# Performance work log

Hardware: AMD Instinct MI355X
Metric: run time of the kernel (lower is better)

## Reference

```python
import jax, jax.numpy as jnp
import numpy as np

D_MODEL = 1024
N_HEADS = 16
D_K = D_MODEL // N_HEADS


def setup_inputs() -> dict:
    key = jax.random.key(0)
    ks = jax.random.split(key, 9)
    s = 1.0 / np.sqrt(D_MODEL)
    x = jax.random.normal(ks[0], (2, 2048, D_MODEL), dtype=jnp.float32)
    Wq = jax.random.normal(ks[1], (D_MODEL, D_MODEL), dtype=jnp.float32) * s
    bq = jnp.zeros((D_MODEL,), jnp.float32)
    Wk = jax.random.normal(ks[2], (D_MODEL, D_MODEL), dtype=jnp.float32) * s
    bk = jnp.zeros((D_MODEL,), jnp.float32)
    Wv = jax.random.normal(ks[3], (D_MODEL, D_MODEL), dtype=jnp.float32) * s
    bv = jnp.zeros((D_MODEL,), jnp.float32)
    Wo = jax.random.normal(ks[4], (D_MODEL, D_MODEL), dtype=jnp.float32) * s
    bo = jnp.zeros((D_MODEL,), jnp.float32)
    return {"x": x, "Wq": Wq, "bq": bq, "Wk": Wk, "bk": bk,
            "Wv": Wv, "bv": bv, "Wo": Wo, "bo": bo}


def reference(x, Wq, bq, Wk, bk, Wv, bv, Wo, bo):
    B, T, C = x.shape
    H, Dk = N_HEADS, D_K
    # QKV projections, reshape to [B, H, T, Dk]
    q = (x @ Wq + bq).reshape(B, T, H, Dk).transpose(0, 2, 1, 3)
    k = (x @ Wk + bk).reshape(B, T, H, Dk).transpose(0, 2, 1, 3)
    v = (x @ Wv + bv).reshape(B, T, H, Dk).transpose(0, 2, 1, 3)
    scale = 1.0 / np.sqrt(Dk).astype(np.float32)
    att = jnp.einsum('bhqd,bhkd->bhqk', q, k) * scale  # [B,H,T,T]
    causal = jnp.tril(jnp.ones((T, T), dtype=bool))
    att = jnp.where(causal, att, -jnp.inf)
    att = jax.nn.softmax(att, axis=-1)
    y = jnp.einsum('bhqk,bhkd->bhqd', att, v)  # [B,H,T,Dk]
    y = y.transpose(0, 2, 1, 3).reshape(B, T, C)
    return y @ Wo + bo
```

## Files before the change

kernel.cpp:

```cpp
#include <hip/hip_runtime.h>
#include <stdint.h>

#define D_MODEL 1024
#define N_HEADS 16
#define D_K     64
#define T_SEQ   2048
#define BATCH   2
#define M_TOT   (BATCH * T_SEQ)
#define QCH     128

typedef __attribute__((ext_vector_type(8))) short  short8;
typedef __attribute__((ext_vector_type(4))) float  f32x4;
typedef __attribute__((ext_vector_type(4))) unsigned short u16x4;

typedef __attribute__((address_space(1))) void gvoid;
typedef __attribute__((address_space(3))) void lvoid;

#define QSCALE 0.18033688011112042f

static __device__ __forceinline__ unsigned short f2bf(float f) {
    union { float f; unsigned u; } v; v.f = f;
    unsigned u = v.u;
    u += 0x7fffu + ((u >> 16) & 1u);
    return (unsigned short)(u >> 16);
}
static __device__ __forceinline__ float bf2f(unsigned short s) {
    union { unsigned u; float f; } v; v.u = ((unsigned)s) << 16;
    return v.f;
}
static __device__ __forceinline__ float fexp2(float x) {
    float r;
    asm("v_exp_f32 %0, %1" : "=v"(r) : "v"(x));
    return r;
}
static __device__ __forceinline__ unsigned cvt_pk_bf16(float lo, float hi) {
    unsigned r;
    asm("v_cvt_pk_bf16_f32 %0, %1, %2" : "=v"(r) : "v"(lo), "v"(hi));
    return r;
}

__global__ void cvt_x(const float* __restrict__ in, unsigned short* __restrict__ out) {
    int idx = blockIdx.x * blockDim.x + threadIdx.x;
    const float4* in4 = (const float4*)in;
    float4 v = in4[idx];
    u16x4 o;
    o.x = f2bf(v.x); o.y = f2bf(v.y); o.z = f2bf(v.z); o.w = f2bf(v.w);
    *(u16x4*)&out[(size_t)idx * 4] = o;
}

__global__ void cvt_w_t(const float* w0, const float* w1, const float* w2, const float* w3,
                        unsigned short* o0, unsigned short* o1, unsigned short* o2, unsigned short* o3) {
    const float* w; unsigned short* o;
    switch (blockIdx.z) {
        case 0: w = w0; o = o0; break;
        case 1: w = w1; o = o1; break;
        case 2: w = w2; o = o2; break;
        default: w = w3; o = o3; break;
    }
    __shared__ float tile[32][33];
    int n0 = blockIdx.x * 32, k0 = blockIdx.y * 32;
    int tx = threadIdx.x, ty = threadIdx.y;
    #pragma unroll
    for (int r = 0; r < 32; r += 8)
        tile[ty + r][tx] = w[(size_t)(k0 + ty + r) * D_MODEL + n0 + tx];
    __syncthreads();
    #pragma unroll
    for (int r = 0; r < 32; r += 8)
        o[(size_t)(n0 + ty + r) * D_MODEL + k0 + tx] = f2bf(tile[tx][ty + r]);
}

__global__ __launch_bounds__(256) void gemm_qkv(const unsigned short* __restrict__ A,
                                                const unsigned short* __restrict__ wq,
                                                const unsigned short* __restrict__ wk,
                                                const unsigned short* __restrict__ wv,
                                                const float* __restrict__ bq,
                                                const float* __restrict__ bk,
                                                const float* __restrict__ bv,
                                                unsigned short* __restrict__ qo,
                                                unsigned short* __restrict__ ko,
                                                unsigned short* __restrict__ vo) {
    const int z = blockIdx.z;
    const unsigned short* Bt = (z == 0) ? wq : (z == 1) ? wk : wv;
    const float* bias = (z == 0) ? bq : (z == 1) ? bk : bv;
    const float alpha = (z == 0) ? QSCALE : 1.0f;

    __shared__ unsigned short lA[128 * 32];
    __shared__ unsigned short lB[128 * 32];
    const int tid  = threadIdx.x;
    const int w    = tid >> 6, lane = tid & 63;
    const int tm   = blockIdx.y, tn = blockIdx.x;
    const int wm   = w & 1, wn = w >> 1;
    const int i16  = lane & 15, g4 = lane >> 4;
    f32x4 acc[4][4] = {};

    const int rA0 = tm * 128, rB0 = tn * 128;
    const int srow = lane >> 2;
    const int skc  = (lane & 3) * 8;

    for (int k0 = 0; k0 < D_MODEL; k0 += 32) {
        #pragma unroll
        for (int is = 0; is < 2; ++is) {
            int c   = is * 4 + w;
            int row = c * 16 + srow;
            __builtin_amdgcn_global_load_lds(
                (gvoid*)(A + (size_t)(rA0 + row) * D_MODEL + k0 + skc),
                (lvoid*)&lA[c * 512], 16, 0, 0);
            __builtin_amdgcn_global_load_lds(
                (gvoid*)(Bt + (size_t)(rB0 + row) * D_MODEL + k0 + skc),
                (lvoid*)&lB[c * 512], 16, 0, 0);
        }
        __syncthreads();
        short8 af[4], bfr[4];
        #pragma unroll
        for (int mi = 0; mi < 4; ++mi)
            af[mi] = *(const short8*)&lA[(wm * 64 + mi * 16 + i16) * 32 + g4 * 8];
        #pragma unroll
        for (int ni = 0; ni < 4; ++ni)
            bfr[ni] = *(const short8*)&lB[(wn * 64 + ni * 16 + i16) * 32 + g4 * 8];
        #pragma unroll
        for (int mi = 0; mi < 4; ++mi)
            #pragma unroll
            for (int ni = 0; ni < 4; ++ni)
                acc[mi][ni] = __builtin_amdgcn_mfma_f32_16x16x32_bf16(af[mi], bfr[ni], acc[mi][ni], 0, 0, 0);
        __syncthreads();
    }

    #pragma unroll
    for (int mi = 0; mi < 4; ++mi)
        #pragma unroll
        for (int ni = 0; ni < 4; ++ni) {
            int col = tn * 128 + wn * 64 + ni * 16 + i16;
            float bv2 = bias[col];
            #pragma unroll
            for (int r = 0; r < 4; ++r) {
                int row = tm * 128 + wm * 64 + mi * 16 + g4 * 4 + r;
                float val = (acc[mi][ni][r] + bv2) * alpha;
                int b = row >> 11, t = row & (T_SEQ - 1);
                int h = col >> 6,  d = col & (D_K - 1);
                unsigned short bfv = f2bf(val);
                if (z == 2)
                    vo[(((size_t)(b * N_HEADS + h)) * D_K + d) * T_SEQ + t] = bfv;
                else if (z == 1)
                    ko[(((size_t)(b * N_HEADS + h)) * T_SEQ + t) * D_K + d] = bfv;
                else
                    qo[(((size_t)(b * N_HEADS + h)) * T_SEQ + t) * D_K + d] = bfv;
            }
        }
}

__global__ __launch_bounds__(256) void gemm_out(const unsigned short* __restrict__ A,
                                                const unsigned short* __restrict__ Bt,
                                                const float* __restrict__ bias,
                                                float* __restrict__ Cout) {
    __shared__ unsigned short lA[128 * 32];
    __shared__ unsigned short lB[128 * 32];
    const int tid  = threadIdx.x;
    const int w    = tid >> 6, lane = tid & 63;
    const int tm   = blockIdx.y, tn = blockIdx.x;
    const int wm   = w & 1, wn = w >> 1;
    const int i16  = lane & 15, g4 = lane >> 4;
    f32x4 acc[4][4] = {};

    const int rA0 = tm * 128, rB0 = tn * 128;
    const int srow = lane >> 2;
    const int skc  = (lane & 3) * 8;

    for (int k0 = 0; k0 < D_MODEL; k0 += 32) {
        #pragma unroll
        for (int is = 0; is < 2; ++is) {
            int c   = is * 4 + w;
            int row = c * 16 + srow;
            __builtin_amdgcn_global_load_lds(
                (gvoid*)(A + (size_t)(rA0 + row) * D_MODEL + k0 + skc),
                (lvoid*)&lA[c * 512], 16, 0, 0);
            __builtin_amdgcn_global_load_lds(
                (gvoid*)(Bt + (size_t)(rB0 + row) * D_MODEL + k0 + skc),
                (lvoid*)&lB[c * 512], 16, 0, 0);
        }
        __syncthreads();
        short8 af[4], bfr[4];
        #pragma unroll
        for (int mi = 0; mi < 4; ++mi)
            af[mi] = *(const short8*)&lA[(wm * 64 + mi * 16 + i16) * 32 + g4 * 8];
        #pragma unroll
        for (int ni = 0; ni < 4; ++ni)
            bfr[ni] = *(const short8*)&lB[(wn * 64 + ni * 16 + i16) * 32 + g4 * 8];
        #pragma unroll
        for (int mi = 0; mi < 4; ++mi)
            #pragma unroll
            for (int ni = 0; ni < 4; ++ni)
                acc[mi][ni] = __builtin_amdgcn_mfma_f32_16x16x32_bf16(af[mi], bfr[ni], acc[mi][ni], 0, 0, 0);
        __syncthreads();
    }

    #pragma unroll
    for (int mi = 0; mi < 4; ++mi)
        #pragma unroll
        for (int ni = 0; ni < 4; ++ni) {
            int col = tn * 128 + wn * 64 + ni * 16 + i16;
            float bv2 = bias[col];
            #pragma unroll
            for (int r = 0; r < 4; ++r) {
                int row = tm * 128 + wm * 64 + mi * 16 + g4 * 4 + r;
                Cout[(size_t)row * D_MODEL + col] = acc[mi][ni][r] + bv2;
            }
        }
}

__global__ __launch_bounds__(256) void flash4(const unsigned short* __restrict__ q,
                                              const unsigned short* __restrict__ k,
                                              const unsigned short* __restrict__ vt,
                                              unsigned short* __restrict__ opart,
                                              float* __restrict__ lws) {
    __shared__ unsigned short lK[2][128 * 64];
    __shared__ unsigned short lV[2][64 * 128];
    __shared__ unsigned short lP[4][16 * 64];
    const int tid  = threadIdx.x;
    const int w    = tid >> 6, lane = tid & 63;
    const int i16  = lane & 15, g4 = lane >> 4;
    const int l8   = lane & 7,  g8 = lane >> 3;
    const int bx   = blockIdx.x;
    const int h    = bx & 1;
    const int bh   = (bx >> 1) & 31;
    const int p    = bx >> 6;

    const unsigned short* kp = k  + (size_t)bh * T_SEQ * D_K;
    const unsigned short* vp = vt + (size_t)bh * D_K * T_SEQ;
    unsigned short* Pw = &lP[w][0];
    const int swz  = (i16 & 7) << 3;
    const int ksrc = (l8 ^ g8) << 3;

    const int b = bh >> 4, hh = bh & 15;
    unsigned short* op = opart + (size_t)h * ((size_t)M_TOT * D_MODEL);

    auto stage = [&](int buf, int t128) {
        const int kvb = t128 * 128;
        #pragma unroll
        for (int i = 0; i < 4; ++i) {
            const int ch  = w * 4 + i;
            const int row = ch * 8 + g8;
            __builtin_amdgcn_global_load_lds(
                (gvoid*)(kp + (size_t)(kvb + row) * D_K + ksrc),
                (lvoid*)&lK[buf][ch * 512], 16, 0, 0);
        }
        #pragma unroll
        for (int i = 0; i < 4; ++i) {
            const int ch  = w * 4 + i;
            const int row = ch * 4 + (lane >> 4);
            const int u   = (lane & 15) ^ (row & 7);
            __builtin_amdgcn_global_load_lds(
                (gvoid*)(vp + (size_t)row * T_SEQ + kvb + u * 8),
                (lvoid*)&lV[buf][ch * 512], 16, 0, 0);
        }
    };

    #pragma unroll 1
    for (int ci = 0; ci < 2; ++ci) {
        const int c   = ci ? p : (15 - p);
        const int q0w = c * QCH + w * 32;
        const int cnt = (c >= h) ? ((c - h) >> 1) + 1 : 0;

        const unsigned short* qp = q + ((size_t)bh * T_SEQ + q0w) * D_K;
        short8 qf[2][2];
        #pragma unroll
        for (int qt = 0; qt < 2; ++qt)
            #pragma unroll
            for (int ks = 0; ks < 2; ++ks)
                qf[qt][ks] = *(const short8*)&qp[(qt * 16 + i16) * D_K + ks * 32 + g4 * 8];

        f32x4 o[2][4] = {};
        float l[2] = {0.f, 0.f};

        if (cnt > 0) stage(0, h);
        __syncthreads();

        for (int it = 0; it < cnt; ++it) {
            const int cur = it & 1;
            const int t   = h + 2 * it;
            if (it + 1 < cnt) stage(cur ^ 1, t + 2);

            #pragma unroll
            for (int sub = 0; sub < 2; ++sub) {
                const int kv0 = t * 128 + sub * 64;
                if (kv0 > q0w + 31) continue;
                const bool act0 = (kv0 <= q0w + 15);
                const unsigned short* Kc = &lK[cur][sub * 64 * 64];

                f32x4 s[4][2] = {};
                __builtin_amdgcn_s_setprio(1);
                #pragma unroll
                for (int ks = 0; ks < 2; ++ks)
                    #pragma unroll
                    for (int kt = 0; kt < 4; ++kt) {
                        short8 ka = *(const short8*)&Kc[(kt * 16 + i16) * 64 + ((ks * 32 + g4 * 8) ^ swz)];
                        if (act0)
                            s[kt][0] = __builtin_amdgcn_mfma_f32_16x16x32_bf16(ka, qf[0][ks], s[kt][0], 0, 0, 0);
                        s[kt][1] = __builtin_amdgcn_mfma_f32_16x16x32_bf16(ka, qf[1][ks], s[kt][1], 0, 0, 0);
                    }
                __builtin_amdgcn_s_setprio(0);

                #pragma unroll
                for (int qt = 0; qt < 2; ++qt) {
                    if (qt == 0 && !act0) continue;
                    const int qrow = q0w + qt * 16 + i16;
                    const bool diag = (kv0 + 63 > q0w + qt * 16);
                    float ps = 0.f;
                    unsigned pk[8];
                    #pragma unroll
                    for (int kt = 0; kt < 4; ++kt) {
                        f32x4 sc = s[kt][qt];
                        if (diag) {
                            #pragma unroll
                            for (int r = 0; r < 4; ++r)
                                if (kv0 + kt * 16 + g4 * 4 + r > qrow) sc[r] = -3e38f;
                        }
                        float p0 = fexp2(sc[0]), p1 = fexp2(sc[1]);
                        float p2 = fexp2(sc[2]), p3 = fexp2(sc[3]);
                        ps += (p0 + p1) + (p2 + p3);
                        pk[kt * 2]     = cvt_pk_bf16(p0, p1);
                        pk[kt * 2 + 1] = cvt_pk_bf16(p2, p3);
                    }
                    l[qt] += ps;
                    #pragma unroll
                    for (int kt = 0; kt < 4; ++kt) {
                        uint2 v2; v2.x = pk[kt * 2]; v2.y = pk[kt * 2 + 1];
                        *(uint2*)&Pw[i16 * 64 + ((kt * 16 + g4 * 4) ^ swz)] = v2;
                    }
                    short8 pB0 = *(const short8*)&Pw[i16 * 64 + (( 0 + g4 * 8) ^ swz)];
                    short8 pB1 = *(const short8*)&Pw[i16 * 64 + ((32 + g4 * 8) ^ swz)];
                    __builtin_amdgcn_s_setprio(1);
                    #pragma unroll
                    for (int dt = 0; dt < 4; ++dt) {
                        short8 va0 = *(const short8*)&lV[cur][(dt * 16 + i16) * 128 + ((sub * 64 +  0 + g4 * 8) ^ swz)];
                        short8 va1 = *(const short8*)&lV[cur][(dt * 16 + i16) * 128 + ((sub * 64 + 32 + g4 * 8) ^ swz)];
                        o[qt][dt] = __builtin_amdgcn_mfma_f32_16x16x32_bf16(va0, pB0, o[qt][dt], 0, 0, 0);
                        o[qt][dt] = __builtin_amdgcn_mfma_f32_16x16x32_bf16(va1, pB1, o[qt][dt], 0, 0, 0);
                    }
                    __builtin_amdgcn_s_setprio(0);
                }
            }
            __syncthreads();
        }

        #pragma unroll
        for (int qt = 0; qt < 2; ++qt) {
            float lt = l[qt] + __shfl_xor(l[qt], 16);
            lt += __shfl_xor(lt, 32);
            const int trow = q0w + qt * 16 + i16;
            if (g4 == 0)
                lws[((size_t)h * 32 + bh) * T_SEQ + trow] = lt;
            #pragma unroll
            for (int dt = 0; dt < 4; ++dt) {
                u16x4 ov;
                ov.x = f2bf(o[qt][dt][0]);
                ov.y = f2bf(o[qt][dt][1]);
                ov.z = f2bf(o[qt][dt][2]);
                ov.w = f2bf(o[qt][dt][3]);
                *(u16x4*)&op[((size_t)(b * T_SEQ) + trow) * D_MODEL + hh * D_K + dt * 16 + g4 * 4] = ov;
            }
        }
    }
}

__global__ __launch_bounds__(256) void merge_halves(const unsigned short* __restrict__ op,
                                                    const float* __restrict__ lws,
                                                    unsigned short* __restrict__ y) {
    const int idx = blockIdx.x * 256 + threadIdx.x;
    const int gl  = idx * 8;
    const int row = gl >> 10;
    const int col = gl & 1023;
    const int b = row >> 11, t = row & (T_SEQ - 1), h = col >> 6;
    const float l0 = lws[((size_t)(b * 16 + h)) * T_SEQ + t];
    const float l1 = lws[((size_t)(32 + b * 16 + h)) * T_SEQ + t];
    const float inv = 1.0f / (l0 + l1);
    short8 a = *(const short8*)&op[gl];
    short8 cc = *(const short8*)&op[(size_t)M_TOT * D_MODEL + gl];
    short8 r;
    #pragma unroll
    for (int j = 0; j < 8; ++j) {
        float f = bf2f((unsigned short)a[j]) + bf2f((unsigned short)cc[j]);
        r[j] = (short)f2bf(f * inv);
    }
    *(short8*)&y[gl] = r;
}

extern "C" void kernel_launch(void* const* d_in, const int* in_sizes, int n_in,
                              void* d_out, int out_size, void* d_ws, size_t ws_size,
                              hipStream_t stream) {
    const float* x  = (const float*)d_in[0];
    const float* Wq = (const float*)d_in[1];
    const float* bq = (const float*)d_in[2];
    const float* Wk = (const float*)d_in[3];
    const float* bk = (const float*)d_in[4];
    const float* Wv = (const float*)d_in[5];
    const float* bv = (const float*)d_in[6];
    const float* Wo = (const float*)d_in[7];
    const float* bo = (const float*)d_in[8];

    uint8_t* ws = (uint8_t*)d_ws;
    const size_t MB = (size_t)1 << 20;
    unsigned short* xb  = (unsigned short*)(ws);
    unsigned short* wqt = (unsigned short*)(ws + 8  * MB);
    unsigned short* wkt = (unsigned short*)(ws + 10 * MB);
    unsigned short* wvt = (unsigned short*)(ws + 12 * MB);
    unsigned short* wot = (unsigned short*)(ws + 14 * MB);
    unsigned short* qb  = (unsigned short*)(ws + 16 * MB);
    unsigned short* kb  = (unsigned short*)(ws + 24 * MB);
    unsigned short* vtb = (unsigned short*)(ws + 32 * MB);
    float* lws = (float*)(ws + 8 * MB);

    cvt_x<<<4096, 256, 0, stream>>>(x, xb);
    cvt_w_t<<<dim3(32, 32, 4), dim3(32, 8), 0, stream>>>(Wq, Wk, Wv, Wo, wqt, wkt, wvt, wot);

    dim3 ggrid(D_MODEL / 128, M_TOT / 128, 3);
    gemm_qkv<<<ggrid, 256, 0, stream>>>(xb, wqt, wkt, wvt, bq, bk, bv, qb, kb, vtb);

    flash4<<<512, 256, 0, stream>>>(qb, kb, vtb, (unsigned short*)d_out, lws);
    merge_halves<<<2048, 256, 0, stream>>>((const unsigned short*)d_out, lws, xb);

    gemm_out<<<dim3(D_MODEL / 128, M_TOT / 128), 256, 0, stream>>>(xb, wot, bo, (float*)d_out);
}
```

Measured before the change: 121.3 us.

## Run both causal query chunks concurrently in 512-thread flash blocks; remap GEMM blocks

The attention kernel now launches 512-thread blocks. Eight waves handle the two paired query chunks (c and 15-c) at the same time instead of one after the other, and they share 64-row K/V tiles loaded once per iteration. Waves whose causal range has ended sit idle at the barriers. Both GEMMs switch to a 1D grid whose block index is remapped so that consecutive blocks land on different XCDs. This is meant to improve L2 locality and spread load across the chiplets, with the risk of more barrier overhead per KV tile.

```diff
diff --git a/kernel.cpp b/kernel.cpp
--- a/kernel.cpp
+++ b/kernel.cpp
@@ -79,7 +79,12 @@
                                                 unsigned short* __restrict__ qo,
                                                 unsigned short* __restrict__ ko,
                                                 unsigned short* __restrict__ vo) {
-    const int z = blockIdx.z;
+    const int nb   = (blockIdx.x & 7) * 96 + (blockIdx.x >> 3);
+    const int tn   = nb & 7;
+    const int rest = nb >> 3;
+    const int tm   = rest & 31;
+    const int z    = rest >> 5;
+
     const unsigned short* Bt = (z == 0) ? wq : (z == 1) ? wk : wv;
     const float* bias = (z == 0) ? bq : (z == 1) ? bk : bv;
     const float alpha = (z == 0) ? QSCALE : 1.0f;
@@ -88,7 +93,6 @@
     __shared__ unsigned short lB[128 * 32];
     const int tid  = threadIdx.x;
     const int w    = tid >> 6, lane = tid & 63;
-    const int tm   = blockIdx.y, tn = blockIdx.x;
     const int wm   = w & 1, wn = w >> 1;
     const int i16  = lane & 15, g4 = lane >> 4;
     f32x4 acc[4][4] = {};
@@ -152,11 +156,14 @@
                                                 const unsigned short* __restrict__ Bt,
                                                 const float* __restrict__ bias,
                                                 float* __restrict__ Cout) {
+    const int nb = (blockIdx.x & 7) * 32 + (blockIdx.x >> 3);
+    const int tn = nb & 7;
+    const int tm = nb >> 3;
+
     __shared__ unsigned short lA[128 * 32];
     __shared__ unsigned short lB[128 * 32];
     const int tid  = threadIdx.x;
     const int w    = tid >> 6, lane = tid & 63;
-    const int tm   = blockIdx.y, tn = blockIdx.x;
     const int wm   = w & 1, wn = w >> 1;
     const int i16  = lane & 15, g4 = lane >> 4;
     f32x4 acc[4][4] = {};
@@ -207,157 +214,142 @@
         }
 }
 
-__global__ __launch_bounds__(256) void flash4(const unsigned short* __restrict__ q,
-                                              const unsigned short* __restrict__ k,
-                                              const unsigned short* __restrict__ vt,
-                                              unsigned short* __restrict__ opart,
-                                              float* __restrict__ lws) {
-    __shared__ unsigned short lK[2][128 * 64];
-    __shared__ unsigned short lV[2][64 * 128];
-    __shared__ unsigned short lP[4][16 * 64];
+__global__ __launch_bounds__(512, 4) void flash5(const unsigned short* __restrict__ q,
+                                                 const unsigned short* __restrict__ k,
+                                                 const unsigned short* __restrict__ vt,
+                                                 unsigned short* __restrict__ opart,
+                                                 float* __restrict__ lws) {
+    __shared__ unsigned short lK[2][64 * 64];
+    __shared__ unsigned short lV[2][64 * 64];
+    __shared__ unsigned short lP[8][16 * 64];
     const int tid  = threadIdx.x;
     const int w    = tid >> 6, lane = tid & 63;
     const int i16  = lane & 15, g4 = lane >> 4;
     const int l8   = lane & 7,  g8 = lane >> 3;
-    const int bx   = blockIdx.x;
-    const int h    = bx & 1;
-    const int bh   = (bx >> 1) & 31;
-    const int p    = bx >> 6;
+
+    const int nb = (blockIdx.x & 7) * 64 + (blockIdx.x >> 3);
+    const int p  = nb & 7;
+    const int h  = (nb >> 3) & 1;
+    const int bh = nb >> 4;
+    const int w4 = w & 3;
+    const int c  = (w >> 2) ? p : (15 - p);
+    const int q0w = c * QCH + w4 * 32;
+    const int cnt = 16 - p;
 
     const unsigned short* kp = k  + (size_t)bh * T_SEQ * D_K;
     const unsigned short* vp = vt + (size_t)bh * D_K * T_SEQ;
+    const unsigned short* qp = q  + ((size_t)bh * T_SEQ + q0w) * D_K;
     unsigned short* Pw = &lP[w][0];
-    const int swz  = (i16 & 7) << 3;
-    const int ksrc = (l8 ^ g8) << 3;
+    const int swz = (i16 & 7) << 3;
+
+    const int srow = tid >> 3;
+    const int sco  = (l8 ^ g8) << 3;
+
+    short8 qf[2][2];
+    #pragma unroll
+    for (int qt = 0; qt < 2; ++qt)
+        #pragma unroll
+        for (int ks = 0; ks < 2; ++ks)
+            qf[qt][ks] = *(const short8*)&qp[(qt * 16 + i16) * D_K + ks * 32 + g4 * 8];
+
+    f32x4 o[2][4] = {};
+    float l[2] = {0.f, 0.f};
+
+    auto stage = [&](int buf, int kv0s) {
+        __builtin_amdgcn_global_load_lds(
+            (gvoid*)(kp + (size_t)(kv0s + srow) * D_K + sco),
+            (lvoid*)&lK[buf][(size_t)tid * 8], 16, 0, 0);
+        __builtin_amdgcn_global_load_lds(
+            (gvoid*)(vp + (size_t)srow * T_SEQ + kv0s + sco),
+            (lvoid*)&lV[buf][(size_t)tid * 8], 16, 0, 0);
+    };
+
+    stage(0, h * 64);
+    __syncthreads();
+
+    for (int it = 0; it < cnt; ++it) {
+        const int cur = it & 1;
+        const int kv0 = (h + 2 * it) * 64;
+        if (it + 1 < cnt) stage(cur ^ 1, kv0 + 128);
+
+        if (kv0 <= q0w + 31) {
+            const bool act0 = (kv0 <= q0w + 15);
+            const unsigned short* Kc = &lK[cur][0];
+            const unsigned short* Vc = &lV[cur][0];
+
+            f32x4 s[4][2] = {};
+            __builtin_amdgcn_s_setprio(1);
+            #pragma unroll
+            for (int ks = 0; ks < 2; ++ks)
+                #pragma unroll
+                for (int kt = 0; kt < 4; ++kt) {
+                    short8 ka = *(const short8*)&Kc[(kt * 16 + i16) * 64 + ((ks * 32 + g4 * 8) ^ swz)];
+                    if (act0)
+                        s[kt][0] = __builtin_amdgcn_mfma_f32_16x16x32_bf16(ka, qf[0][ks], s[kt][0], 0, 0, 0);
+                    s[kt][1] = __builtin_amdgcn_mfma_f32_16x16x32_bf16(ka, qf[1][ks], s[kt][1], 0, 0, 0);
+                }
+            __builtin_amdgcn_s_setprio(0);
+
+            #pragma unroll
+            for (int qt = 0; qt < 2; ++qt) {
+                if (qt == 0 && !act0) continue;
+                const int qrow = q0w + qt * 16 + i16;
+                const bool diag = (kv0 + 63 > q0w + qt * 16);
+                float ps = 0.f;
+                unsigned pk[8];
+                #pragma unroll
+                for (int kt = 0; kt < 4; ++kt) {
+                    f32x4 sc = s[kt][qt];
+                    if (diag) {
+                        #pragma unroll
+                        for (int r = 0; r < 4; ++r)
+                            if (kv0 + kt * 16 + g4 * 4 + r > qrow) sc[r] = -3e38f;
+                    }
+                    float p0 = fexp2(sc[0]), p1 = fexp2(sc[1]);
+                    float p2 = fexp2(sc[2]), p3 = fexp2(sc[3]);
+                    ps += (p0 + p1) + (p2 + p3);
+                    pk[kt * 2]     = cvt_pk_bf16(p0, p1);
+                    pk[kt * 2 + 1] = cvt_pk_bf16(p2, p3);
+                }
+                l[qt] += ps;
+                #pragma unroll
+                for (int kt = 0; kt < 4; ++kt) {
+                    uint2 v2; v2.x = pk[kt * 2]; v2.y = pk[kt * 2 + 1];
+                    *(uint2*)&Pw[i16 * 64 + ((kt * 16 + g4 * 4) ^ swz)] = v2;
+                }
+                short8 pB0 = *(const short8*)&Pw[i16 * 64 + (( 0 + g4 * 8) ^ swz)];
+                short8 pB1 = *(const short8*)&Pw[i16 * 64 + ((32 + g4 * 8) ^ swz)];
+                __builtin_amdgcn_s_setprio(1);
+                #pragma unroll
+                for (int dt = 0; dt < 4; ++dt) {
+                    short8 va0 = *(const short8*)&Vc[(dt * 16 + i16) * 64 + (( 0 + g4 * 8) ^ swz)];
+                    short8 va1 = *(const short8*)&Vc[(dt * 16 + i16) * 64 + ((32 + g4 * 8) ^ swz)];
+                    o[qt][dt] = __builtin_amdgcn_mfma_f32_16x16x32_bf16(va0, pB0, o[qt][dt], 0, 0, 0);
+                    o[qt][dt] = __builtin_amdgcn_mfma_f32_16x16x32_bf16(va1, pB1, o[qt][dt], 0, 0, 0);
+                }
+                __builtin_amdgcn_s_setprio(0);
+            }
+        }
+        __syncthreads();
+    }
 
     const int b = bh >> 4, hh = bh & 15;
     unsigned short* op = opart + (size_t)h * ((size_t)M_TOT * D_MODEL);
-
-    auto stage = [&](int buf, int t128) {
-        const int kvb = t128 * 128;
-        #pragma unroll
-        for (int i = 0; i < 4; ++i) {
-            const int ch  = w * 4 + i;
-            const int row = ch * 8 + g8;
-            __builtin_amdgcn_global_load_lds(
-                (gvoid*)(kp + (size_t)(kvb + row) * D_K + ksrc),
-                (lvoid*)&lK[buf][ch * 512], 16, 0, 0);
-        }
-        #pragma unroll
-        for (int i = 0; i < 4; ++i) {
-            const int ch  = w * 4 + i;
-            const int row = ch * 4 + (lane >> 4);
-            const int u   = (lane & 15) ^ (row & 7);
-            __builtin_amdgcn_global_load_lds(
-                (gvoid*)(vp + (size_t)row * T_SEQ + kvb + u * 8),
-                (lvoid*)&lV[buf][ch * 512], 16, 0, 0);
-        }
-    };
-
-    #pragma unroll 1
-    for (int ci = 0; ci < 2; ++ci) {
-        const int c   = ci ? p : (15 - p);
-        const int q0w = c * QCH + w * 32;
-        const int cnt = (c >= h) ? ((c - h) >> 1) + 1 : 0;
-
-        const unsigned short* qp = q + ((size_t)bh * T_SEQ + q0w) * D_K;
-        short8 qf[2][2];
-        #pragma unroll
-        for (int qt = 0; qt < 2; ++qt)
-            #pragma unroll
-            for (int ks = 0; ks < 2; ++ks)
-                qf[qt][ks] = *(const short8*)&qp[(qt * 16 + i16) * D_K + ks * 32 + g4 * 8];
-
-        f32x4 o[2][4] = {};
-        float l[2] = {0.f, 0.f};
-
-        if (cnt > 0) stage(0, h);
-        __syncthreads();
-
-        for (int it = 0; it < cnt; ++it) {
-            const int cur = it & 1;
-            const int t   = h + 2 * it;
-            if (it + 1 < cnt) stage(cur ^ 1, t + 2);
-
-            #pragma unroll
-            for (int sub = 0; sub < 2; ++sub) {
-                const int kv0 = t * 128 + sub * 64;
-                if (kv0 > q0w + 31) continue;
-                const bool act0 = (kv0 <= q0w + 15);
-                const unsigned short* Kc = &lK[cur][sub * 64 * 64];
-
-                f32x4 s[4][2] = {};
-                __builtin_amdgcn_s_setprio(1);
-                #pragma unroll
-                for (int ks = 0; ks < 2; ++ks)
-                    #pragma unroll
-                    for (int kt = 0; kt < 4; ++kt) {
-                        short8 ka = *(const short8*)&Kc[(kt * 16 + i16) * 64 + ((ks * 32 + g4 * 8) ^ swz)];
-                        if (act0)
-                            s[kt][0] = __builtin_amdgcn_mfma_f32_16x16x32_bf16(ka, qf[0][ks], s[kt][0], 0, 0, 0);
-                        s[kt][1] = __builtin_amdgcn_mfma_f32_16x16x32_bf16(ka, qf[1][ks], s[kt][1], 0, 0, 0);
-                    }
-                __builtin_amdgcn_s_setprio(0);
-
-                #pragma unroll
-                for (int qt = 0; qt < 2; ++qt) {
-                    if (qt == 0 && !act0) continue;
-                    const int qrow = q0w + qt * 16 + i16;
-                    const bool diag = (kv0 + 63 > q0w + qt * 16);
-                    float ps = 0.f;
-                    unsigned pk[8];
-                    #pragma unroll
-                    for (int kt = 0; kt < 4; ++kt) {
-                        f32x4 sc = s[kt][qt];
-                        if (diag) {
-                            #pragma unroll
-                            for (int r = 0; r < 4; ++r)
-                                if (kv0 + kt * 16 + g4 * 4 + r > qrow) sc[r] = -3e38f;
-                        }
-                        float p0 = fexp2(sc[0]), p1 = fexp2(sc[1]);
-                        float p2 = fexp2(sc[2]), p3 = fexp2(sc[3]);
-                        ps += (p0 + p1) + (p2 + p3);
-                        pk[kt * 2]     = cvt_pk_bf16(p0, p1);
-                        pk[kt * 2 + 1] = cvt_pk_bf16(p2, p3);
-                    }
-                    l[qt] += ps;
-                    #pragma unroll
-                    for (int kt = 0; kt < 4; ++kt) {
-                        uint2 v2; v2.x = pk[kt * 2]; v2.y = pk[kt * 2 + 1];
-                        *(uint2*)&Pw[i16 * 64 + ((kt * 16 + g4 * 4) ^ swz)] = v2;
-                    }
-                    short8 pB0 = *(const short8*)&Pw[i16 * 64 + (( 0 + g4 * 8) ^ swz)];
-                    short8 pB1 = *(const short8*)&Pw[i16 * 64 + ((32 + g4 * 8) ^ swz)];
-                    __builtin_amdgcn_s_setprio(1);
-                    #pragma unroll
-                    for (int dt = 0; dt < 4; ++dt) {
-                        short8 va0 = *(const short8*)&lV[cur][(dt * 16 + i16) * 128 + ((sub * 64 +  0 + g4 * 8) ^ swz)];
-                        short8 va1 = *(const short8*)&lV[cur][(dt * 16 + i16) * 128 + ((sub * 64 + 32 + g4 * 8) ^ swz)];
-                        o[qt][dt] = __builtin_amdgcn_mfma_f32_16x16x32_bf16(va0, pB0, o[qt][dt], 0, 0, 0);
-                        o[qt][dt] = __builtin_amdgcn_mfma_f32_16x16x32_bf16(va1, pB1, o[qt][dt], 0, 0, 0);
-                    }
-                    __builtin_amdgcn_s_setprio(0);
-                }
-            }
-            __syncthreads();
-        }
-
-        #pragma unroll
-        for (int qt = 0; qt < 2; ++qt) {
-            float lt = l[qt] + __shfl_xor(l[qt], 16);
-            lt += __shfl_xor(lt, 32);
-            const int trow = q0w + qt * 16 + i16;
-            if (g4 == 0)
-                lws[((size_t)h * 32 + bh) * T_SEQ + trow] = lt;
-            #pragma unroll
-            for (int dt = 0; dt < 4; ++dt) {
-                u16x4 ov;
-                ov.x = f2bf(o[qt][dt][0]);
-                ov.y = f2bf(o[qt][dt][1]);
-                ov.z = f2bf(o[qt][dt][2]);
-                ov.w = f2bf(o[qt][dt][3]);
-                *(u16x4*)&op[((size_t)(b * T_SEQ) + trow) * D_MODEL + hh * D_K + dt * 16 + g4 * 4] = ov;
-            }
+    #pragma unroll
+    for (int qt = 0; qt < 2; ++qt) {
+        float lt = l[qt] + __shfl_xor(l[qt], 16);
+        lt += __shfl_xor(lt, 32);
+        const int trow = q0w + qt * 16 + i16;
+        if (g4 == 0)
+            lws[((size_t)h * 32 + bh) * T_SEQ + trow] = lt;
+        #pragma unroll
+        for (int dt = 0; dt < 4; ++dt) {
+            u16x4 ov;
+            ov.x = f2bf(o[qt][dt][0]);
+            ov.y = f2bf(o[qt][dt][1]);
+            ov.z = f2bf(o[qt][dt][2]);
+            ov.w = f2bf(o[qt][dt][3]);
+            *(u16x4*)&op[((size_t)(b * T_SEQ) + trow) * D_MODEL + hh * D_K + dt * 16 + g4 * 4] = ov;
         }
     }
 }
@@ -412,11 +404,10 @@
     cvt_x<<<4096, 256, 0, stream>>>(x, xb);
     cvt_w_t<<<dim3(32, 32, 4), dim3(32, 8), 0, stream>>>(Wq, Wk, Wv, Wo, wqt, wkt, wvt, wot);
 
-    dim3 ggrid(D_MODEL / 128, M_TOT / 128, 3);
-    gemm_qkv<<<ggrid, 256, 0, stream>>>(xb, wqt, wkt, wvt, bq, bk, bv, qb, kb, vtb);
-
-    flash4<<<512, 256, 0, stream>>>(qb, kb, vtb, (unsigned short*)d_out, lws);
+    gemm_qkv<<<768, 256, 0, stream>>>(xb, wqt, wkt, wvt, bq, bk, bv, qb, kb, vtb);
+
+    flash5<<<512, 512, 0, stream>>>(qb, kb, vtb, (unsigned short*)d_out, lws);
     merge_halves<<<2048, 256, 0, stream>>>((const unsigned short*)d_out, lws, xb);
 
-    gemm_out<<<dim3(D_MODEL / 128, M_TOT / 128), 256, 0, stream>>>(xb, wot, bo, (float*)d_out);
-}
+    gemm_out<<<256, 256, 0, stream>>>(xb, wot, bo, (float*)d_out);
+}
```

Measured after the change: 129.2 us. 1.07x slower.
